# Kernel optimization log

Hardware: AMD Instinct MI355X
Metric: run time of the kernel (lower is better)

The kernel has to match this reference:

```python
import jax, jax.numpy as jnp
import numpy as np

B, LQ, LK, D = 16, 2048, 2048, 64
EPS = 1e-13
KEEP_PROB = 0.8  # fraction of key positions kept in the mask


def setup_inputs() -> dict:
    key = jax.random.key(0)
    kq, kk, kv, km = jax.random.split(key, 4)
    q = jax.random.normal(kq, (B, LQ, D), dtype=jnp.float32)
    k = jax.random.normal(kk, (B, LK, D), dtype=jnp.float32)
    v = jax.random.normal(kv, (B, LK, D), dtype=jnp.float32)
    # binary 0/1 float mask over key positions (ESIM-style padding mask)
    v_mask = (jax.random.uniform(km, (B, LK)) < KEEP_PROB).astype(jnp.float32)
    return {"q": q, "k": k, "v": v, "v_mask": v_mask}


def masked_softmax(scores, mask):
    # ESIM masked_softmax: softmax(scores * mask) * mask, renormalized.
    m = mask[:, None, :]  # [B, 1, Lk] broadcast over query dim
    p = jax.nn.softmax(scores * m, axis=-1) * m
    return p / (jnp.sum(p, axis=-1, keepdims=True) + EPS)


def reference(q, k, v, v_mask):
    scores = jnp.einsum("bqd,bkd->bqk", q, k)  # [B, Lq, Lk]
    attend = masked_softmax(scores, v_mask)
    return jnp.einsum("bqk,bkd->bqd", attend, v)  # [B, Lq, D]
```

## Files before the change

kernel.cpp:

```cpp
#include <hip/hip_runtime.h>
#include <hip/hip_bf16.h>
#include <stdint.h>

#define NB 16
#define SLQ 2048
#define SLK 2048
#define DD 64
#define BQ 128
#define BK 64
#define NT (SLK / BK)
#define QTILES (SLQ / BQ)
#define LOG2E 1.44269504f

typedef _Float16 f16x8 __attribute__((ext_vector_type(8)));
typedef short s16x8 __attribute__((ext_vector_type(8)));
typedef unsigned int u32x4 __attribute__((ext_vector_type(4)));
typedef unsigned short u16x4 __attribute__((ext_vector_type(4)));
typedef float f32x4 __attribute__((ext_vector_type(4)));
typedef float f32x2 __attribute__((ext_vector_type(2)));
typedef float f32x16 __attribute__((ext_vector_type(16)));

typedef __attribute__((address_space(1))) const void gvoid;
typedef __attribute__((address_space(3))) void lvoid;

__device__ __forceinline__ int swzb(int row, int bytecol) {
    return row * 128 + (bytecol ^ ((row & 7) << 4));
}
__device__ __forceinline__ int ldsq(int row, int bytecol) {
    return (row >> 6) * 8192 + swzb(row & 63, bytecol);
}

__device__ __forceinline__ void gload16(const void* g, void* l) {
    __builtin_amdgcn_global_load_lds((gvoid*)g, (lvoid*)l, 16, 0, 0);
}

__device__ __forceinline__ uint16_t f2bf(float f) {
    __bf16 h = (__bf16)f;
    return __builtin_bit_cast(uint16_t, h);
}
__device__ __forceinline__ float bf2f(uint16_t u) {
    uint32_t x = ((uint32_t)u) << 16;
    return __builtin_bit_cast(float, x);
}

__device__ __forceinline__ int sigma16(int x) {
    return (x & ~12) | ((x & 4) << 1) | ((x & 8) >> 1);
}

__device__ __forceinline__ void build_pa(const f32x16& s, s16x8& paA, s16x8& paB) {
    uint32_t w[8];
    #pragma unroll
    for (int i = 0; i < 8; ++i) {
        float p0 = exp2f(s[2 * i]);
        float p1 = exp2f(s[2 * i + 1]);
        w[i] = (uint32_t)f2bf(p0) | ((uint32_t)f2bf(p1) << 16);
    }
    u32x4 wa = {w[0], w[1], w[2], w[3]};
    u32x4 wb = {w[4], w[5], w[6], w[7]};
    paA = __builtin_bit_cast(s16x8, wa);
    paB = __builtin_bit_cast(s16x8, wb);
}

__global__ __launch_bounds__(256)
void prep_all(const float* __restrict__ q, const float* __restrict__ k,
              const float* __restrict__ v, const float* __restrict__ vm,
              char* __restrict__ qs, char* __restrict__ ks,
              char* __restrict__ vts, uint16_t* __restrict__ mb16) {
    const int bid = blockIdx.x;
    if (bid < 1024) {
        const int tl = bid & 511;
        const bool isq = bid < 512;
        const float sc = isq ? LOG2E : 1.0f;
        const float* src = (isq ? q : k) + (size_t)tl * (BK * DD);
        char* dst = (isq ? qs : ks) + (size_t)tl * (BK * DD * 2);
        #pragma unroll
        for (int it = 0; it < 2; ++it) {
            int c = threadIdx.x + it * 256;
            int row = c >> 3, col8 = c & 7;
            f32x4 a  = *(const f32x4*)(src + row * DD + col8 * 8);
            f32x4 b2 = *(const f32x4*)(src + row * DD + col8 * 8 + 4);
            f16x8 h;
            #pragma unroll
            for (int j = 0; j < 4; ++j) {
                h[j] = (_Float16)(a[j] * sc);
                h[4 + j] = (_Float16)(b2[j] * sc);
            }
            *(f16x8*)(dst + swzb(row, col8 * 16)) = h;
        }
    } else if (bid < 1536) {
        const int tl = bid - 1024;
        const float* src = v + (size_t)tl * (BK * DD);
        const float* msk = vm + (size_t)tl * BK;
        char* dst = vts + (size_t)tl * (BK * DD * 2);
        const int d = threadIdx.x & 63;
        #pragma unroll
        for (int it = 0; it < 2; ++it) {
            int key8 = (threadIdx.x >> 6) + it * 4;
            s16x8 h;
            #pragma unroll
            for (int j = 0; j < 8; ++j) {
                int kp = key8 * 8 + j;
                int sk = (kp & ~15) | sigma16(kp & 15);
                float mv = msk[sk];
                h[j] = (short)f2bf((mv != 0.f) ? src[sk * DD + d] : 0.f);
            }
            *(s16x8*)(dst + swzb(d, key8 * 16)) = h;
        }
    } else {
        int i = (bid - 1536) * 1024 + threadIdx.x * 4;
        f32x4 m = *(const f32x4*)(vm + i);
        u16x4 o;
        #pragma unroll
        for (int j = 0; j < 4; ++j) o[j] = (m[j] != 0.f) ? (uint16_t)0x3F80 : (uint16_t)0;
        int pos = (i & ~15) | sigma16(i & 15);
        *(u16x4*)(mb16 + pos) = o;
    }
}

__global__ __launch_bounds__(256, 3)
void attn_fwd(const char* __restrict__ qs, const char* __restrict__ ks,
              const char* __restrict__ vts, const uint16_t* __restrict__ mb16,
              float* __restrict__ po, float* __restrict__ pl,
              float* __restrict__ out, int nsp)
{
    __shared__ __align__(16) char lq[BQ * DD * 2];
    __shared__ __align__(16) char lk[2][BK * DD * 2];
    __shared__ __align__(16) char lv[2][BK * DD * 2];

    const int tid  = threadIdx.x;
    const int lane = tid & 63;
    const int w    = tid >> 6;
    const int lh   = lane >> 5;
    const int lr   = lane & 31;

    const int G = 256 * nsp;
    int wg = blockIdx.x;
    wg = (wg & 7) * (G >> 3) + (wg >> 3);
    const int qt   = wg & 15;
    const int rest = wg >> 4;
    const int sp   = rest % nsp;
    const int b    = rest / nsp;

    const int qq = NT / nsp, rm = NT % nsp;
    const int t0  = sp * qq + (sp < rm ? sp : rm);
    const int cnt = qq + (sp < rm ? 1 : 0);

    const char* qtile = qs  + (size_t)(b * 32 + qt * 2) * 8192;
    const char* kbase = ks  + (size_t)(b * 32 + t0) * 8192;
    const char* vbase = vts + (size_t)(b * 32 + t0) * 8192;
    const uint16_t* mkbase = mb16 + (size_t)b * SLK + t0 * BK;

    #pragma unroll
    for (int i = 0; i < 4; ++i) {
        int ch = w * 4 + i;
        gload16(qtile + ch * 1024 + lane * 16, lq + ch * 1024);
    }
    #pragma unroll
    for (int i = 0; i < 2; ++i) {
        int ch = w * 2 + i;
        gload16(kbase + ch * 1024 + lane * 16, lk[0] + ch * 1024);
        gload16(vbase + ch * 1024 + lane * 16, lv[0] + ch * 1024);
    }
    asm volatile("s_waitcnt vmcnt(0)" ::: "memory");
    __syncthreads();

    f16x8 qf[4];
    #pragma unroll
    for (int kd = 0; kd < 4; ++kd)
        qf[kd] = *(const f16x8*)(lq + ldsq(w * 32 + lr, kd * 32 + lh * 16));

    f32x16 oacc0 = (f32x16)(0.0f), oacc1 = (f32x16)(0.0f), rsacc = (f32x16)(0.0f);

    int buf = 0;
    for (int kt = 0; kt < cnt; ++kt) {
        s16x8 mf[4];
        #pragma unroll
        for (int kk = 0; kk < 4; ++kk)
            mf[kk] = *(const s16x8*)(mkbase + kt * BK + kk * 16 + lh * 8);

        if (kt + 1 < cnt) {
            const char* kg = kbase + (size_t)(kt + 1) * 8192;
            const char* vg = vbase + (size_t)(kt + 1) * 8192;
            #pragma unroll
            for (int i = 0; i < 2; ++i) {
                int ch = w * 2 + i;
                gload16(kg + ch * 1024 + lane * 16, lk[buf ^ 1] + ch * 1024);
                gload16(vg + ch * 1024 + lane * 16, lv[buf ^ 1] + ch * 1024);
            }
        }

        f32x16 s0 = (f32x16)(0.0f), s1 = (f32x16)(0.0f);
        #pragma unroll
        for (int kd = 0; kd < 4; ++kd) {
            f16x8 kf0 = *(const f16x8*)(lk[buf] + swzb(lr,      kd * 32 + lh * 16));
            f16x8 kf1 = *(const f16x8*)(lk[buf] + swzb(32 + lr, kd * 32 + lh * 16));
            s0 = __builtin_amdgcn_mfma_f32_32x32x16_f16(kf0, qf[kd], s0, 0, 0, 0);
            s1 = __builtin_amdgcn_mfma_f32_32x32x16_f16(kf1, qf[kd], s1, 0, 0, 0);
        }

        s16x8 pa[4];
        build_pa(s0, pa[0], pa[1]);
        build_pa(s1, pa[2], pa[3]);

        #pragma unroll
        for (int kk = 0; kk < 4; ++kk)
            rsacc = __builtin_amdgcn_mfma_f32_32x32x16_bf16(pa[kk], mf[kk], rsacc, 0, 0, 0);

        #pragma unroll
        for (int kk = 0; kk < 4; ++kk) {
            s16x8 vf0 = *(const s16x8*)(lv[buf] + swzb(lr,      kk * 32 + lh * 16));
            s16x8 vf1 = *(const s16x8*)(lv[buf] + swzb(32 + lr, kk * 32 + lh * 16));
            oacc0 = __builtin_amdgcn_mfma_f32_32x32x16_bf16(pa[kk], vf0, oacc0, 0, 0, 0);
            oacc1 = __builtin_amdgcn_mfma_f32_32x32x16_bf16(pa[kk], vf1, oacc1, 0, 0, 0);
        }

        asm volatile("s_waitcnt vmcnt(0)" ::: "memory");
        __syncthreads();
        buf ^= 1;
    }

    if (nsp == 1) {
        float* ob = out + ((size_t)b * SLQ + (size_t)qt * BQ) * DD;
        #pragma unroll
        for (int r = 0; r < 16; ++r) {
            int row = w * 32 + (r & 3) + 8 * (r >> 2) + 4 * lh;
            float inv = 1.f / (rsacc[r] + 1e-13f);
            ob[row * DD + lr]      = oacc0[r] * inv;
            ob[row * DD + 32 + lr] = oacc1[r] * inv;
        }
    } else {
        float* pob = po + (size_t)wg * (BQ * DD);
        #pragma unroll
        for (int r = 0; r < 16; ++r) {
            int row = w * 32 + (r & 3) + 8 * (r >> 2) + 4 * lh;
            pob[row * DD + lr]      = oacc0[r];
            pob[row * DD + 32 + lr] = oacc1[r];
            if (lr == 0) pl[(size_t)wg * BQ + row] = rsacc[r];
        }
    }
}

__global__ __launch_bounds__(256)
void merge_k(const float* __restrict__ po, const float* __restrict__ pl,
             float* __restrict__ out, int nsp) {
    const int t  = blockIdx.x;
    const int b  = t >> 4, qt = t & 15;
    const int i0 = (b * nsp) * 16 + qt;
    const int r0 = threadIdx.x >> 4;
    const int c4 = (threadIdx.x & 15) * 4;
    float* ob = out + ((size_t)b * SLQ + (size_t)qt * BQ) * DD;
    for (int rr = 0; rr < BQ; rr += 16) {
        int r = r0 + rr;
        float l = 1e-13f;
        f32x4 acc = (f32x4){0.f, 0.f, 0.f, 0.f};
        for (int s = 0; s < nsp; ++s) {
            int idx = i0 + s * 16;
            l += pl[(size_t)idx * BQ + r];
            f32x4 a = *(const f32x4*)(po + (size_t)idx * (BQ * DD) + r * DD + c4);
            acc += a;
        }
        float inv = 1.f / l;
        f32x4 o;
        #pragma unroll
        for (int j = 0; j < 4; ++j) o[j] = acc[j] * inv;
        *(f32x4*)(ob + r * DD + c4) = o;
    }
}

__global__ __launch_bounds__(256, 2)
void attn_fallback(const float* __restrict__ q, const float* __restrict__ k,
                   const float* __restrict__ v, const float* __restrict__ vm,
                   float* __restrict__ out)
{
    __shared__ __align__(16) char lqh[64 * DD * 2];
    __shared__ __align__(16) char lql[64 * DD * 2];
    __shared__ __align__(16) char lkh[BK * DD * 2];
    __shared__ __align__(16) char lkl[BK * DD * 2];
    __shared__ __align__(16) char lvt[DD * BK * 2];
    __shared__ __align__(16) char lpp[64 * BK * 2];
    __shared__ float lmask[BK];

    const int tid  = threadIdx.x;
    const int lane = tid & 63;
    const int w    = tid >> 6;
    const int lg   = lane >> 4;
    const int lm   = lane & 15;

    const int b  = blockIdx.y;
    const int qt = blockIdx.x;

    const float* qb = q + ((size_t)b * SLQ + (size_t)qt * 64) * DD;
    const float* kb = k + (size_t)b * SLK * DD;
    const float* vb = v + (size_t)b * SLK * DD;
    const float* mb = vm + (size_t)b * SLK;

    #pragma unroll
    for (int it = 0; it < 2; ++it) {
        int c = tid + it * 256;
        int row = c >> 3, col8 = c & 7;
        f32x4 a  = *(const f32x4*)(qb + row * DD + col8 * 8);
        f32x4 bb = *(const f32x4*)(qb + row * DD + col8 * 8 + 4);
        s16x8 h, l;
        #pragma unroll
        for (int j = 0; j < 4; ++j) {
            uint16_t hh = f2bf(a[j]);
            h[j] = (short)hh; l[j] = (short)f2bf(a[j] - bf2f(hh));
            uint16_t hb = f2bf(bb[j]);
            h[4 + j] = (short)hb; l[4 + j] = (short)f2bf(bb[j] - bf2f(hb));
        }
        *(s16x8*)(lqh + swzb(row, col8 * 16)) = h;
        *(s16x8*)(lql + swzb(row, col8 * 16)) = l;
    }
    __syncthreads();

    s16x8 qfh[2], qfl[2];
    #pragma unroll
    for (int kc = 0; kc < 2; ++kc) {
        qfh[kc] = *(const s16x8*)(lqh + swzb(w * 16 + lm, kc * 64 + lg * 16));
        qfl[kc] = *(const s16x8*)(lql + swzb(w * 16 + lm, kc * 64 + lg * 16));
    }

    float mrow[4], lrow[4];
    f32x4 oacc[4];
    #pragma unroll
    for (int i = 0; i < 4; ++i) { mrow[i] = -1e30f; lrow[i] = 0.f; }
    #pragma unroll
    for (int d = 0; d < 4; ++d) oacc[d] = (f32x4){0.f, 0.f, 0.f, 0.f};

    for (int kt = 0; kt < NT; ++kt) {
        __syncthreads();
        const float* ks2 = kb + (size_t)kt * BK * DD;
        const float* vs = vb + (size_t)kt * BK * DD;

        #pragma unroll
        for (int it = 0; it < 2; ++it) {
            int c = tid + it * 256;
            int row = c >> 3, col8 = c & 7;
            f32x4 a  = *(const f32x4*)(ks2 + row * DD + col8 * 8);
            f32x4 bb = *(const f32x4*)(ks2 + row * DD + col8 * 8 + 4);
            s16x8 h, l;
            #pragma unroll
            for (int j = 0; j < 4; ++j) {
                uint16_t hh = f2bf(a[j]);
                h[j] = (short)hh; l[j] = (short)f2bf(a[j] - bf2f(hh));
                uint16_t hb = f2bf(bb[j]);
                h[4 + j] = (short)hb; l[4 + j] = (short)f2bf(bb[j] - bf2f(hb));
            }
            *(s16x8*)(lkh + swzb(row, col8 * 16)) = h;
            *(s16x8*)(lkl + swzb(row, col8 * 16)) = l;
        }
        #pragma unroll
        for (int it = 0; it < 8; ++it) {
            int c = tid + it * 256;
            int key = c >> 5, dp = (c & 31) * 2;
            f32x2 a = *(const f32x2*)(vs + key * DD + dp);
            *(uint16_t*)(lvt + swzb(dp,     key * 2)) = f2bf(a[0]);
            *(uint16_t*)(lvt + swzb(dp + 1, key * 2)) = f2bf(a[1]);
        }
        if (tid < BK) lmask[tid] = mb[kt * BK + tid];
        __syncthreads();

        f32x4 s[4];
        #pragma unroll
        for (int f = 0; f < 4; ++f) s[f] = (f32x4){0.f, 0.f, 0.f, 0.f};
        #pragma unroll
        for (int f = 0; f < 4; ++f) {
            #pragma unroll
            for (int kc = 0; kc < 2; ++kc) {
                s16x8 kfh = *(const s16x8*)(lkh + swzb(f * 16 + lm, kc * 64 + lg * 16));
                s16x8 kfl = *(const s16x8*)(lkl + swzb(f * 16 + lm, kc * 64 + lg * 16));
                s[f] = __builtin_amdgcn_mfma_f32_16x16x32_bf16(qfh[kc], kfh, s[f], 0, 0, 0);
                s[f] = __builtin_amdgcn_mfma_f32_16x16x32_bf16(qfh[kc], kfl, s[f], 0, 0, 0);
                s[f] = __builtin_amdgcn_mfma_f32_16x16x32_bf16(qfl[kc], kfh, s[f], 0, 0, 0);
            }
        }

        float mv[4];
        #pragma unroll
        for (int f = 0; f < 4; ++f) mv[f] = lmask[f * 16 + lm];

        float pmax[4];
        #pragma unroll
        for (int i = 0; i < 4; ++i) {
            float x = -1e30f;
            #pragma unroll
            for (int f = 0; f < 4; ++f) {
                float sv = (mv[f] != 0.f) ? s[f][i] : -1e30f;
                s[f][i] = sv;
                x = fmaxf(x, sv);
            }
            #pragma unroll
            for (int off = 1; off < 16; off <<= 1)
                x = fmaxf(x, __shfl_xor(x, off, 64));
            pmax[i] = x;
        }

        float scl[4];
        #pragma unroll
        for (int i = 0; i < 4; ++i) {
            float mn = fmaxf(mrow[i], pmax[i]);
            scl[i] = __expf(mrow[i] - mn);
            mrow[i] = mn;
        }
        float rs[4] = {0.f, 0.f, 0.f, 0.f};
        #pragma unroll
        for (int f = 0; f < 4; ++f) {
            #pragma unroll
            for (int i = 0; i < 4; ++i) {
                float p = __expf(s[f][i] - mrow[i]);
                s[f][i] = p;
                rs[i] += p;
            }
        }
        #pragma unroll
        for (int i = 0; i < 4; ++i) {
            #pragma unroll
            for (int off = 1; off < 16; off <<= 1)
                rs[i] += __shfl_xor(rs[i], off, 64);
            lrow[i] = lrow[i] * scl[i] + rs[i];
        }
        #pragma unroll
        for (int d = 0; d < 4; ++d)
            #pragma unroll
            for (int i = 0; i < 4; ++i)
                oacc[d][i] *= scl[i];

        #pragma unroll
        for (int f = 0; f < 4; ++f)
            #pragma unroll
            for (int i = 0; i < 4; ++i)
                *(uint16_t*)(lpp + swzb(w * 16 + lg * 4 + i, (f * 16 + lm) * 2)) = f2bf(s[f][i]);
        __syncthreads();

        #pragma unroll
        for (int kc = 0; kc < 2; ++kc) {
            s16x8 pf = *(const s16x8*)(lpp + swzb(w * 16 + lm, kc * 64 + lg * 16));
            #pragma unroll
            for (int d = 0; d < 4; ++d) {
                s16x8 vf = *(const s16x8*)(lvt + swzb(d * 16 + lm, kc * 64 + lg * 16));
                oacc[d] = __builtin_amdgcn_mfma_f32_16x16x32_bf16(pf, vf, oacc[d], 0, 0, 0);
            }
        }
    }

    float* ob = out + ((size_t)b * SLQ + (size_t)qt * 64) * DD;
    #pragma unroll
    for (int i = 0; i < 4; ++i) {
        float inv = 1.f / (lrow[i] + 1e-13f);
        int row = w * 16 + lg * 4 + i;
        #pragma unroll
        for (int d = 0; d < 4; ++d)
            ob[row * DD + d * 16 + lm] = oacc[d][i] * inv;
    }
}

extern "C" void kernel_launch(void* const* d_in, const int* in_sizes, int n_in,
                              void* d_out, int out_size, void* d_ws, size_t ws_size,
                              hipStream_t stream) {
    const float* q  = (const float*)d_in[0];
    const float* k  = (const float*)d_in[1];
    const float* v  = (const float*)d_in[2];
    const float* vm = (const float*)d_in[3];
    float* out = (float*)d_out;

    const size_t TB     = (size_t)NB * SLK * DD * 2;
    const size_t MB     = (size_t)NB * SLK * 2;
    const size_t PL_PER = (size_t)NB * QTILES * BQ * 4;
    const size_t PO_PER = (size_t)NB * QTILES * BQ * DD * 4;
    const size_t base = 3 * TB + MB;

    int nsp = 0;
    for (int c = 3; c >= 1; --c) {
        if (ws_size >= base + (size_t)c * (PL_PER + PO_PER)) { nsp = c; break; }
    }
    if (nsp == 0) {
        if (ws_size >= base) nsp = 1;
        else {
            dim3 grid(SLQ / 64, NB);
            attn_fallback<<<grid, dim3(256), 0, stream>>>(q, k, v, vm, out);
            return;
        }
    }

    char*     qs   = (char*)d_ws;
    char*     ks   = qs + TB;
    char*     vts  = ks + TB;
    uint16_t* mb16 = (uint16_t*)(vts + TB);
    float*    pl   = (float*)((char*)mb16 + MB);
    float*    po   = (float*)((char*)pl + (size_t)nsp * PL_PER);

    prep_all<<<dim3(1568), dim3(256), 0, stream>>>(q, k, v, vm, qs, ks, vts, mb16);
    attn_fwd<<<dim3(256 * nsp), dim3(256), 0, stream>>>(qs, ks, vts, mb16, po, pl, out, nsp);
    if (nsp > 1)
        merge_k<<<dim3(NB * QTILES), dim3(256), 0, stream>>>(po, pl, out, nsp);
}
```

Before: 57.23 us.

## Triple-buffer K/V/mask tiles via LDS, raise MFMA priority, store partials as bf16

Replaces the double-buffered K/V pipeline with a three-stage ring in shared memory that prefetches two tiles ahead. The mask tile is also staged through LDS with async loads, and the Q buffer is reused as the third stage after Q is read into registers. The loop waits with partial vmcnt counts and raw barriers instead of a full drain each iteration, which should hide more global-load latency. MFMA sections are wrapped in s_setprio, and split-K partial outputs are written and merged as bf16 to halve that traffic, at some cost in accuracy.

```diff
diff --git a/kernel.cpp b/kernel.cpp
--- a/kernel.cpp
+++ b/kernel.cpp
@@ -32,6 +32,9 @@
 
 __device__ __forceinline__ void gload16(const void* g, void* l) {
     __builtin_amdgcn_global_load_lds((gvoid*)g, (lvoid*)l, 16, 0, 0);
+}
+__device__ __forceinline__ void gload4(const void* g, void* l) {
+    __builtin_amdgcn_global_load_lds((gvoid*)g, (lvoid*)l, 4, 0, 0);
 }
 
 __device__ __forceinline__ uint16_t f2bf(float f) {
@@ -120,12 +123,10 @@
 __global__ __launch_bounds__(256, 3)
 void attn_fwd(const char* __restrict__ qs, const char* __restrict__ ks,
               const char* __restrict__ vts, const uint16_t* __restrict__ mb16,
-              float* __restrict__ po, float* __restrict__ pl,
+              uint16_t* __restrict__ po, float* __restrict__ pl,
               float* __restrict__ out, int nsp)
 {
-    __shared__ __align__(16) char lq[BQ * DD * 2];
-    __shared__ __align__(16) char lk[2][BK * DD * 2];
-    __shared__ __align__(16) char lv[2][BK * DD * 2];
+    __shared__ __align__(16) char bufs[3][16640];
 
     const int tid  = threadIdx.x;
     const int lane = tid & 63;
@@ -150,74 +151,95 @@
     const char* vbase = vts + (size_t)(b * 32 + t0) * 8192;
     const uint16_t* mkbase = mb16 + (size_t)b * SLK + t0 * BK;
 
+#define STAGE(kt, bf) do {                                                      \
+        const char* kg_ = kbase + (size_t)(kt) * 8192;                          \
+        const char* vg_ = vbase + (size_t)(kt) * 8192;                          \
+        _Pragma("unroll")                                                       \
+        for (int i_ = 0; i_ < 2; ++i_) {                                        \
+            int ch_ = w * 2 + i_;                                               \
+            gload16(kg_ + ch_ * 1024 + lane * 16, bufs[bf] + ch_ * 1024);       \
+            gload16(vg_ + ch_ * 1024 + lane * 16, bufs[bf] + 8192 + ch_ * 1024);\
+        }                                                                       \
+        gload4((const char*)(mkbase + (size_t)(kt) * BK) + (lane & 31) * 4,     \
+               bufs[bf] + 16384);                                               \
+    } while (0)
+
     #pragma unroll
     for (int i = 0; i < 4; ++i) {
         int ch = w * 4 + i;
-        gload16(qtile + ch * 1024 + lane * 16, lq + ch * 1024);
-    }
-    #pragma unroll
-    for (int i = 0; i < 2; ++i) {
-        int ch = w * 2 + i;
-        gload16(kbase + ch * 1024 + lane * 16, lk[0] + ch * 1024);
-        gload16(vbase + ch * 1024 + lane * 16, lv[0] + ch * 1024);
-    }
-    asm volatile("s_waitcnt vmcnt(0)" ::: "memory");
-    __syncthreads();
+        gload16(qtile + ch * 1024 + lane * 16, bufs[2] + ch * 1024);
+    }
+    STAGE(0, 0);
+    if (cnt > 1) {
+        STAGE(1, 1);
+        asm volatile("s_waitcnt vmcnt(5)" ::: "memory");
+    } else {
+        asm volatile("s_waitcnt vmcnt(0)" ::: "memory");
+    }
+    __builtin_amdgcn_s_barrier();
 
     f16x8 qf[4];
     #pragma unroll
     for (int kd = 0; kd < 4; ++kd)
-        qf[kd] = *(const f16x8*)(lq + ldsq(w * 32 + lr, kd * 32 + lh * 16));
+        qf[kd] = *(const f16x8*)(bufs[2] + ldsq(w * 32 + lr, kd * 32 + lh * 16));
+    asm volatile("s_waitcnt lgkmcnt(0)" ::: "memory");
+    __builtin_amdgcn_s_barrier();
 
     f32x16 oacc0 = (f32x16)(0.0f), oacc1 = (f32x16)(0.0f), rsacc = (f32x16)(0.0f);
 
-    int buf = 0;
-    for (int kt = 0; kt < cnt; ++kt) {
+    for (int t = 0; t < cnt; ++t) {
+        const int cur = t % 3;
+        if (t + 2 < cnt) {
+            STAGE(t + 2, (t + 2) % 3);
+            asm volatile("s_waitcnt vmcnt(10)" ::: "memory");
+        } else if (t + 1 < cnt) {
+            asm volatile("s_waitcnt vmcnt(5)" ::: "memory");
+        } else {
+            asm volatile("s_waitcnt vmcnt(0)" ::: "memory");
+        }
+        __builtin_amdgcn_s_barrier();
+
+        const char* kb_ = bufs[cur];
+        const char* vb_ = bufs[cur] + 8192;
+        const char* mb_ = bufs[cur] + 16384;
+
         s16x8 mf[4];
         #pragma unroll
         for (int kk = 0; kk < 4; ++kk)
-            mf[kk] = *(const s16x8*)(mkbase + kt * BK + kk * 16 + lh * 8);
-
-        if (kt + 1 < cnt) {
-            const char* kg = kbase + (size_t)(kt + 1) * 8192;
-            const char* vg = vbase + (size_t)(kt + 1) * 8192;
-            #pragma unroll
-            for (int i = 0; i < 2; ++i) {
-                int ch = w * 2 + i;
-                gload16(kg + ch * 1024 + lane * 16, lk[buf ^ 1] + ch * 1024);
-                gload16(vg + ch * 1024 + lane * 16, lv[buf ^ 1] + ch * 1024);
-            }
-        }
-
+            mf[kk] = *(const s16x8*)(mb_ + kk * 32 + lh * 16);
+
+        __builtin_amdgcn_s_setprio(1);
         f32x16 s0 = (f32x16)(0.0f), s1 = (f32x16)(0.0f);
         #pragma unroll
         for (int kd = 0; kd < 4; ++kd) {
-            f16x8 kf0 = *(const f16x8*)(lk[buf] + swzb(lr,      kd * 32 + lh * 16));
-            f16x8 kf1 = *(const f16x8*)(lk[buf] + swzb(32 + lr, kd * 32 + lh * 16));
+            f16x8 kf0 = *(const f16x8*)(kb_ + swzb(lr,      kd * 32 + lh * 16));
+            f16x8 kf1 = *(const f16x8*)(kb_ + swzb(32 + lr, kd * 32 + lh * 16));
             s0 = __builtin_amdgcn_mfma_f32_32x32x16_f16(kf0, qf[kd], s0, 0, 0, 0);
             s1 = __builtin_amdgcn_mfma_f32_32x32x16_f16(kf1, qf[kd], s1, 0, 0, 0);
         }
+        __builtin_amdgcn_s_setprio(0);
 
         s16x8 pa[4];
         build_pa(s0, pa[0], pa[1]);
         build_pa(s1, pa[2], pa[3]);
 
+        __builtin_amdgcn_s_setprio(1);
         #pragma unroll
         for (int kk = 0; kk < 4; ++kk)
             rsacc = __builtin_amdgcn_mfma_f32_32x32x16_bf16(pa[kk], mf[kk], rsacc, 0, 0, 0);
-
         #pragma unroll
         for (int kk = 0; kk < 4; ++kk) {
-            s16x8 vf0 = *(const s16x8*)(lv[buf] + swzb(lr,      kk * 32 + lh * 16));
-            s16x8 vf1 = *(const s16x8*)(lv[buf] + swzb(32 + lr, kk * 32 + lh * 16));
+            s16x8 vf0 = *(const s16x8*)(vb_ + swzb(lr,      kk * 32 + lh * 16));
+            s16x8 vf1 = *(const s16x8*)(vb_ + swzb(32 + lr, kk * 32 + lh * 16));
             oacc0 = __builtin_amdgcn_mfma_f32_32x32x16_bf16(pa[kk], vf0, oacc0, 0, 0, 0);
             oacc1 = __builtin_amdgcn_mfma_f32_32x32x16_bf16(pa[kk], vf1, oacc1, 0, 0, 0);
         }
-
-        asm volatile("s_waitcnt vmcnt(0)" ::: "memory");
-        __syncthreads();
-        buf ^= 1;
-    }
+        __builtin_amdgcn_s_setprio(0);
+
+        asm volatile("s_waitcnt lgkmcnt(0)" ::: "memory");
+        __builtin_amdgcn_s_barrier();
+    }
+#undef STAGE
 
     if (nsp == 1) {
         float* ob = out + ((size_t)b * SLQ + (size_t)qt * BQ) * DD;
@@ -229,19 +251,19 @@
             ob[row * DD + 32 + lr] = oacc1[r] * inv;
         }
     } else {
-        float* pob = po + (size_t)wg * (BQ * DD);
+        uint16_t* pob = po + (size_t)wg * (BQ * DD);
         #pragma unroll
         for (int r = 0; r < 16; ++r) {
             int row = w * 32 + (r & 3) + 8 * (r >> 2) + 4 * lh;
-            pob[row * DD + lr]      = oacc0[r];
-            pob[row * DD + 32 + lr] = oacc1[r];
+            pob[row * DD + lr]      = f2bf(oacc0[r]);
+            pob[row * DD + 32 + lr] = f2bf(oacc1[r]);
             if (lr == 0) pl[(size_t)wg * BQ + row] = rsacc[r];
         }
     }
 }
 
 __global__ __launch_bounds__(256)
-void merge_k(const float* __restrict__ po, const float* __restrict__ pl,
+void merge_k(const uint16_t* __restrict__ po, const float* __restrict__ pl,
              float* __restrict__ out, int nsp) {
     const int t  = blockIdx.x;
     const int b  = t >> 4, qt = t & 15;
@@ -256,8 +278,9 @@
         for (int s = 0; s < nsp; ++s) {
             int idx = i0 + s * 16;
             l += pl[(size_t)idx * BQ + r];
-            f32x4 a = *(const f32x4*)(po + (size_t)idx * (BQ * DD) + r * DD + c4);
-            acc += a;
+            u16x4 a = *(const u16x4*)(po + (size_t)idx * (BQ * DD) + r * DD + c4);
+            #pragma unroll
+            for (int j = 0; j < 4; ++j) acc[j] += bf2f(a[j]);
         }
         float inv = 1.f / l;
         f32x4 o;
@@ -466,7 +489,7 @@
     const size_t TB     = (size_t)NB * SLK * DD * 2;
     const size_t MB     = (size_t)NB * SLK * 2;
     const size_t PL_PER = (size_t)NB * QTILES * BQ * 4;
-    const size_t PO_PER = (size_t)NB * QTILES * BQ * DD * 4;
+    const size_t PO_PER = (size_t)NB * QTILES * BQ * DD * 2;
     const size_t base = 3 * TB + MB;
 
     int nsp = 0;
@@ -487,7 +510,7 @@
     char*     vts  = ks + TB;
     uint16_t* mb16 = (uint16_t*)(vts + TB);
     float*    pl   = (float*)((char*)mb16 + MB);
-    float*    po   = (float*)((char*)pl + (size_t)nsp * PL_PER);
+    uint16_t* po   = (uint16_t*)((char*)pl + (size_t)nsp * PL_PER);
 
     prep_all<<<dim3(1568), dim3(256), 0, stream>>>(q, k, v, vm, qs, ks, vts, mb16);
     attn_fwd<<<dim3(256 * nsp), dim3(256), 0, stream>>>(qs, ks, vts, mb16, po, pl, out, nsp);
```

Result: slower. 58.66 us (+2.5%).
